# Optimization experiments

Hardware: AMD Instinct MI355X
Metric: run time of the kernel (lower is better)

Reference implementation:

```python
import jax, jax.numpy as jnp
import numpy as np

CAP = 15.0
EPS = 1e-6
NUM_HEADS = 16
HEAD_DIM = 64

def _rmsnorm(x, w):
    xf = x.astype(jnp.float32)
    var = jnp.mean(xf * xf, axis=-1, keepdims=True)
    return w * (xf * jax.lax.rsqrt(var + EPS)).astype(x.dtype)

def _gate(g):
    # sigmoid(soft_cap(g)) with cap 15
    return jax.nn.sigmoid(CAP * jnp.tanh(g / CAP))

def setup_inputs() -> dict:
    key = jax.random.key(0)
    ks = jax.random.split(key, 4)
    B, S, D = 4, 2048, 1024
    H, Dh = NUM_HEADS, HEAD_DIM
    return {
        "x": jax.random.normal(ks[0], (B, S, D), jnp.float32),
        "hidden_state": jnp.zeros((B, H, Dh, Dh), jnp.float32),
        "w_rms": jnp.ones((D,), jnp.float32),
        "w_qkv": jax.random.normal(ks[1], (D, 3 * H * Dh), jnp.float32) * 0.02,
        "w_gate": jax.random.normal(ks[2], (D, 3 * H), jnp.float32) * 0.02,
        "w_out": jax.random.normal(ks[3], (D, D), jnp.float32) * 0.02,
    }

def reference(x, hidden_state, w_rms, w_qkv, w_gate, w_out):
    B, S, D = x.shape
    H, Dh = NUM_HEADS, HEAD_DIM
    residual = x
    xn = _rmsnorm(x, w_rms)
    qkv = (xn @ w_qkv).reshape(B, S, 3, H, Dh)
    q, k, v = qkv[:, :, 0], qkv[:, :, 1], qkv[:, :, 2]  # [B,S,H,Dh]
    gates = _gate((xn @ w_gate).reshape(B, S, 3, H))
    i_g, f_g, o_g = gates[:, :, 0], gates[:, :, 1], gates[:, :, 2]  # [B,S,H]

    # time-major for scan: [S,B,H,...]
    def tm(a):
        return jnp.moveaxis(a, 1, 0)

    def step(state, inp):
        qt, kt, vt, it, ft, ot = inp  # [B,H,Dh]/[B,H]
        kv = kt[..., :, None] * vt[..., None, :]            # [B,H,Dh,Dh]
        state = ft[..., None, None] * state + it[..., None, None] * kv
        h = jnp.einsum('bhd,bhde->bhe', qt, state) * ot[..., None]
        return state, h

    _, h_seq = jax.lax.scan(step, hidden_state,
                            (tm(q), tm(k), tm(v), tm(i_g), tm(f_g), tm(o_g)))
    out = jnp.moveaxis(h_seq, 0, 1).reshape(B, S, H * Dh) @ w_out
    return residual + out
```

## Files before the change

kernel.cpp:

```cpp
#include <hip/hip_runtime.h>
#include <math.h>

typedef unsigned short u16;
typedef unsigned int   u32;
typedef __bf16 bf16x8 __attribute__((ext_vector_type(8)));
typedef float  f32x4  __attribute__((ext_vector_type(4)));

#define NBATCH 4
#define SEQ    2048
#define DIM    1024
#define NH     16
#define BH     64
#define NC     32
#define ROWS   8192
#define N1     3200

__device__ __forceinline__ u16 f2bf(float f) {
  u32 u = __builtin_bit_cast(u32, f);
  u32 r = u + 0x7fffu + ((u >> 16) & 1u);
  return (u16)(r >> 16);
}
__device__ __forceinline__ float bf2f(u16 h) {
  return __builtin_bit_cast(float, (u32)h << 16);
}

__device__ __forceinline__ void gl2lds16(const u16* g, u16* l) {
  __builtin_amdgcn_global_load_lds(
      (const __attribute__((address_space(1))) u32*)g,
      (__attribute__((address_space(3))) u32*)l, 16, 0, 0);
}

__global__ __launch_bounds__(256) void transpose_w(const float* __restrict__ W,
                                                   u16* __restrict__ Bt, int K, int N) {
  __shared__ float tile[32][33];
  const int n0 = blockIdx.x * 32, k0 = blockIdx.y * 32;
  const int tx = threadIdx.x, ty = threadIdx.y;
  #pragma unroll
  for (int i = 0; i < 4; i++)
    tile[ty + i * 8][tx] = W[(size_t)(k0 + ty + i * 8) * N + n0 + tx];
  __syncthreads();
  #pragma unroll
  for (int i = 0; i < 4; i++)
    Bt[(size_t)(n0 + ty + i * 8) * K + k0 + tx] = f2bf(tile[tx][ty + i * 8]);
}

__global__ __launch_bounds__(256) void fill_gateW(const float* __restrict__ wg,
                                                  u16* __restrict__ Bt) {
  const int g = blockIdx.x;
  const int tid = threadIdx.x;
  #pragma unroll
  for (int kk = 0; kk < 4; kk++) {
    const int k = kk * 256 + tid;
    u16 v = 0;
    if (g < 48) v = f2bf(wg[(size_t)k * 48 + g]);
    Bt[(size_t)(3072 + g) * 1024 + k] = v;
  }
}

__global__ __launch_bounds__(256) void rmsnorm_k(const float* __restrict__ x,
                                                 const float* __restrict__ w,
                                                 u16* __restrict__ xn) {
  const int row = blockIdx.x, tid = threadIdx.x;
  const float4 xv = *(const float4*)&x[(size_t)row * 1024 + tid * 4];
  float ss = xv.x * xv.x + xv.y * xv.y + xv.z * xv.z + xv.w * xv.w;
  #pragma unroll
  for (int off = 32; off > 0; off >>= 1) ss += __shfl_down(ss, off);
  __shared__ float red[4];
  if ((tid & 63) == 0) red[tid >> 6] = ss;
  __syncthreads();
  const float tot = red[0] + red[1] + red[2] + red[3];
  const float scale = rsqrtf(tot * (1.0f / 1024.0f) + 1e-6f);
  const float4 wv = *(const float4*)&w[tid * 4];
  const u16 o0 = f2bf(xv.x * scale * wv.x), o1 = f2bf(xv.y * scale * wv.y);
  const u16 o2 = f2bf(xv.z * scale * wv.z), o3 = f2bf(xv.w * scale * wv.w);
  uint2 ov;
  ov.x = (u32)o0 | ((u32)o1 << 16);
  ov.y = (u32)o2 | ((u32)o3 << 16);
  *(uint2*)&xn[(size_t)row * 1024 + tid * 4] = ov;
}

__device__ __forceinline__ void gemm_core256(const u16* __restrict__ A, const u16* __restrict__ Bt,
                                             int K, int rowBase, int colBase,
                                             u16* As, u16* Bs, f32x4 (&acc)[4][4]) {
  const int tid = threadIdx.x;
  const int lane = tid & 63;
  const int q = lane >> 4, m16 = lane & 15;
  const int wave = tid >> 6;
  const int wm = wave & 3, wn = wave >> 2;
  const u16* gA[4]; u16* lA[4];
  const u16* gB[2]; u16* lB[2];
  #pragma unroll
  for (int j = 0; j < 4; j++) {
    const int c = tid + j * 512;
    gA[j] = &A[(size_t)(rowBase + (c >> 3)) * K + (c & 7) * 8];
    lA[j] = As + c * 8;
  }
  #pragma unroll
  for (int j = 0; j < 2; j++) {
    const int c = tid + j * 512;
    gB[j] = &Bt[(size_t)(colBase + (c >> 3)) * K + (c & 7) * 8];
    lB[j] = Bs + c * 8;
  }
  for (int kb = 0; kb < K / 64; ++kb) {
    __syncthreads();
    #pragma unroll
    for (int j = 0; j < 4; j++) { gl2lds16(gA[j], lA[j]); gA[j] += 64; }
    #pragma unroll
    for (int j = 0; j < 2; j++) { gl2lds16(gB[j], lB[j]); gB[j] += 64; }
    __syncthreads();
    #pragma unroll
    for (int ks = 0; ks < 2; ks++) {
      bf16x8 af[4], bfr[4];
      #pragma unroll
      for (int mi = 0; mi < 4; mi++)
        af[mi] = *(const bf16x8*)&As[(wm * 64 + mi * 16 + m16) * 64 + ks * 32 + q * 8];
      #pragma unroll
      for (int ni = 0; ni < 4; ni++)
        bfr[ni] = *(const bf16x8*)&Bs[(wn * 64 + ni * 16 + m16) * 64 + ks * 32 + q * 8];
      #pragma unroll
      for (int mi = 0; mi < 4; mi++)
        #pragma unroll
        for (int ni = 0; ni < 4; ni++)
          acc[mi][ni] = __builtin_amdgcn_mfma_f32_16x16x32_bf16(af[mi], bfr[ni], acc[mi][ni], 0, 0, 0);
    }
  }
}

__device__ __forceinline__ void gemm_core128(const u16* __restrict__ A, const u16* __restrict__ Bt,
                                             int K, int rowBase, int colBase,
                                             u16* As, u16* Bs, f32x4 (&acc)[4][4]) {
  const int tid = threadIdx.x;
  const int lane = tid & 63;
  const int q = lane >> 4, m16 = lane & 15;
  const int wave = tid >> 6;
  const int wm = wave & 1, wn = wave >> 1;
  const u16* gA[4]; u16* lA[4];
  const u16* gB[4]; u16* lB[4];
  #pragma unroll
  for (int j = 0; j < 4; j++) {
    const int c = tid + j * 256;
    gA[j] = &A[(size_t)(rowBase + (c >> 3)) * K + (c & 7) * 8];
    lA[j] = As + c * 8;
    gB[j] = &Bt[(size_t)(colBase + (c >> 3)) * K + (c & 7) * 8];
    lB[j] = Bs + c * 8;
  }
  for (int kb = 0; kb < K / 64; ++kb) {
    __syncthreads();
    #pragma unroll
    for (int j = 0; j < 4; j++) { gl2lds16(gA[j], lA[j]); gA[j] += 64; }
    #pragma unroll
    for (int j = 0; j < 4; j++) { gl2lds16(gB[j], lB[j]); gB[j] += 64; }
    __syncthreads();
    #pragma unroll
    for (int ks = 0; ks < 2; ks++) {
      bf16x8 af[4], bfr[4];
      #pragma unroll
      for (int mi = 0; mi < 4; mi++)
        af[mi] = *(const bf16x8*)&As[(wm * 64 + mi * 16 + m16) * 64 + ks * 32 + q * 8];
      #pragma unroll
      for (int ni = 0; ni < 4; ni++)
        bfr[ni] = *(const bf16x8*)&Bs[(wn * 64 + ni * 16 + m16) * 64 + ks * 32 + q * 8];
      #pragma unroll
      for (int mi = 0; mi < 4; mi++)
        #pragma unroll
        for (int ni = 0; ni < 4; ni++)
          acc[mi][ni] = __builtin_amdgcn_mfma_f32_16x16x32_bf16(af[mi], bfr[ni], acc[mi][ni], 0, 0, 0);
    }
  }
}

__global__ __launch_bounds__(512, 4) void gemm_qkv(const u16* __restrict__ A, const u16* __restrict__ Bt,
                                                   u16* __restrict__ Qb, u16* __restrict__ Kb,
                                                   u16* __restrict__ Vb, float* __restrict__ gates) {
  __shared__ __attribute__((aligned(16))) u16 As[256 * 64];
  __shared__ __attribute__((aligned(16))) u16 Bs[128 * 64];
  f32x4 acc[4][4] = {};
  const int rowBase = blockIdx.x * 256, colBase = blockIdx.y * 128;
  gemm_core256(A, Bt, 1024, rowBase, colBase, As, Bs, acc);
  const int tid = threadIdx.x;
  const int lane = tid & 63, wave = tid >> 6;
  const int q = lane >> 4, m16 = lane & 15;
  const int wm = wave & 3, wn = wave >> 2;
  __syncthreads();
  if (colBase < 3072) {
    const int which = colBase >> 10;
    u16* dstBase = (which == 0) ? Qb : ((which == 1) ? Kb : Vb);
    const int b = rowBase >> 11;
    const int h = ((colBase & 1023) >> 6) + wn;
    const int tRow0 = (rowBase & 2047) + wm * 64;
    u16* scratch = As + wave * 1024;
    u16* headBase = dstBase + ((size_t)(b * 16 + h)) * 2048 * 64;
    const int rr = lane >> 2, co = (lane & 3) * 16;
    #pragma unroll
    for (int mi = 0; mi < 4; mi++) {
      #pragma unroll
      for (int ni = 0; ni < 4; ni++)
        #pragma unroll
        for (int r = 0; r < 4; r++)
          scratch[(q * 4 + r) * 64 + ni * 16 + m16] = f2bf(acc[mi][ni][r]);
      const uint4 d0 = *(const uint4*)&scratch[rr * 64 + co];
      const uint4 d1 = *(const uint4*)&scratch[rr * 64 + co + 8];
      u16* gp = headBase + (size_t)(tRow0 + mi * 16 + rr) * 64 + co;
      *(uint4*)gp = d0;
      *(uint4*)(gp + 8) = d1;
    }
  } else {
    #pragma unroll
    for (int ni = 0; ni < 4; ni++) {
      const int c2 = wn * 64 + ni * 16 + m16;
      if (c2 < 48) {
        const int which = c2 >> 4, hh = c2 & 15;
        #pragma unroll
        for (int mi = 0; mi < 4; mi++)
          #pragma unroll
          for (int r = 0; r < 4; r++) {
            const int grow = rowBase + wm * 64 + mi * 16 + q * 4 + r;
            const int b = grow >> 11, t = grow & 2047;
            const float v = acc[mi][ni][r];
            const float g = 1.0f / (1.0f + expf(-(15.0f * tanhf(v * (1.0f / 15.0f)))));
            gates[((size_t)which * 64 + (b * 16 + hh)) * 2048 + t] = g;
          }
      }
    }
  }
}

__global__ __launch_bounds__(256, 4) void gemm_out(const u16* __restrict__ A, const u16* __restrict__ Bt,
                                                   const float* __restrict__ resid,
                                                   float* __restrict__ out) {
  __shared__ __attribute__((aligned(16))) u16 As[128 * 64];
  __shared__ __attribute__((aligned(16))) u16 Bs[128 * 64];
  f32x4 acc[4][4] = {};
  const int rowBase = blockIdx.x * 128, colBase = blockIdx.y * 128;
  gemm_core128(A, Bt, 1024, rowBase, colBase, As, Bs, acc);
  const int tid = threadIdx.x;
  const int lane = tid & 63, wave = tid >> 6;
  const int q = lane >> 4, m16 = lane & 15;
  const int wm = wave & 1, wn = wave >> 1;
  #pragma unroll
  for (int mi = 0; mi < 4; mi++)
    #pragma unroll
    for (int ni = 0; ni < 4; ni++)
      #pragma unroll
      for (int r = 0; r < 4; r++) {
        const int grow = rowBase + wm * 64 + mi * 16 + q * 4 + r;
        const int gcol = colBase + wn * 64 + ni * 16 + m16;
        const size_t idx = (size_t)grow * 1024 + gcol;
        out[idx] = acc[mi][ni][r] + resid[idx];
      }
}

__global__ __launch_bounds__(64) void la_k(const float* __restrict__ gates,
                                           float* __restrict__ la) {
  const int bh = blockIdx.x >> 5, c = blockIdx.x & 31, lane = threadIdx.x;
  const int t = c * 64 + lane;
  float x = logf(gates[(size_t)(64 + bh) * 2048 + t]);
  #pragma unroll
  for (int off = 1; off < 64; off <<= 1) {
    const float y = __shfl_up(x, off);
    if (lane >= off) x += y;
  }
  la[(size_t)bh * 2048 + t] = x;
}

__global__ __launch_bounds__(256) void passA_k(const u16* __restrict__ Qb, const u16* __restrict__ Kb,
                                               const u16* __restrict__ Vb,
                                               const float* __restrict__ gates,
                                               const float* __restrict__ la,
                                               float* __restrict__ Mbuf, u16* __restrict__ hseq) {
  __shared__ u16 Ql[64][72], Kl[64][72], KTl[64][72], VTl[64][72], Pl[64][72];
  __shared__ float laS[64], iS[64];
  const int tid = threadIdx.x;
  const int bh = blockIdx.x >> 5, c = blockIdx.x & 31;
  const int lane = tid & 63, w = tid >> 6;
  const int q = lane >> 4, m16 = lane & 15;
  const size_t base = ((size_t)bh * 2048 + c * 64) * 64;
  const int tbase = bh * 2048 + c * 64;

  {
    const int s = tid >> 2, db = (tid & 3) * 16;
    if (tid < 64) {
      laS[tid] = la[tbase + tid];
      iS[tid] = gates[(size_t)bh * 2048 + c * 64 + tid];
    }
    const float la_s = la[tbase + s];
    const float i_s = gates[(size_t)bh * 2048 + c * 64 + s];
    const float la63 = la[tbase + 63];
    const float wk = expf(la63 - la_s) * i_s;
    const uint4 q0 = *(const uint4*)&Qb[base + s * 64 + db];
    const uint4 q1 = *(const uint4*)&Qb[base + s * 64 + db + 8];
    *(uint4*)&Ql[s][db] = q0;
    *(uint4*)&Ql[s][db + 8] = q1;
    const uint4 k0 = *(const uint4*)&Kb[base + s * 64 + db];
    const uint4 k1 = *(const uint4*)&Kb[base + s * 64 + db + 8];
    *(uint4*)&Kl[s][db] = k0;
    *(uint4*)&Kl[s][db + 8] = k1;
    u16 ktmp[16];
    *(uint4*)&ktmp[0] = k0;
    *(uint4*)&ktmp[8] = k1;
    #pragma unroll
    for (int j = 0; j < 16; j++) KTl[db + j][s] = f2bf(wk * bf2f(ktmp[j]));
    const uint4 v0 = *(const uint4*)&Vb[base + s * 64 + db];
    const uint4 v1 = *(const uint4*)&Vb[base + s * 64 + db + 8];
    u16 vtmp[16];
    *(uint4*)&vtmp[0] = v0;
    *(uint4*)&vtmp[8] = v1;
    #pragma unroll
    for (int j = 0; j < 16; j++) VTl[db + j][s] = vtmp[j];
  }
  __syncthreads();

  f32x4 pacc[4] = {};
  #pragma unroll
  for (int ks = 0; ks < 2; ks++) {
    const bf16x8 aq = *(const bf16x8*)&Ql[w * 16 + m16][ks * 32 + q * 8];
    #pragma unroll
    for (int ni = 0; ni < 4; ni++) {
      const bf16x8 bk = *(const bf16x8*)&Kl[ni * 16 + m16][ks * 32 + q * 8];
      pacc[ni] = __builtin_amdgcn_mfma_f32_16x16x32_bf16(aq, bk, pacc[ni], 0, 0, 0);
    }
  }
  #pragma unroll
  for (int ni = 0; ni < 4; ni++)
    #pragma unroll
    for (int r = 0; r < 4; r++) {
      const int tt = w * 16 + q * 4 + r, ss = ni * 16 + m16;
      float Wts = 0.0f;
      if (ss <= tt) Wts = expf(laS[tt] - laS[ss]) * iS[ss];
      Pl[tt][ss] = f2bf(pacc[ni][r] * Wts);
    }
  __syncthreads();

  f32x4 hacc[4] = {}, macc[4] = {};
  #pragma unroll
  for (int ks = 0; ks < 2; ks++) {
    const bf16x8 ap = *(const bf16x8*)&Pl[w * 16 + m16][ks * 32 + q * 8];
    const bf16x8 ak = *(const bf16x8*)&KTl[w * 16 + m16][ks * 32 + q * 8];
    #pragma unroll
    for (int ni = 0; ni < 4; ni++) {
      const bf16x8 bv = *(const bf16x8*)&VTl[ni * 16 + m16][ks * 32 + q * 8];
      hacc[ni] = __builtin_amdgcn_mfma_f32_16x16x32_bf16(ap, bv, hacc[ni], 0, 0, 0);
      macc[ni] = __builtin_amdgcn_mfma_f32_16x16x32_bf16(ak, bv, macc[ni], 0, 0, 0);
    }
  }
  const int b = bh >> 4, h = bh & 15;
  #pragma unroll
  for (int ni = 0; ni < 4; ni++)
    #pragma unroll
    for (int r = 0; r < 4; r++) {
      const int tt = w * 16 + q * 4 + r, e = ni * 16 + m16;
      const int tg = c * 64 + tt;
      hseq[((size_t)b * 2048 + tg) * 1024 + h * 64 + e] = f2bf(hacc[ni][r]);
      Mbuf[(((size_t)bh * 32 + c) * 64 + tt) * 64 + e] = macc[ni][r];
    }
}

__global__ __launch_bounds__(256) void passB_k(float* __restrict__ Mbuf,
                                               const float* __restrict__ hidden,
                                               const float* __restrict__ la) {
  const int bh = blockIdx.x >> 4;
  const int e = (blockIdx.x & 15) * 256 + threadIdx.x;
  __shared__ float Gs[32];
  if (threadIdx.x < 32)
    Gs[threadIdx.x] = expf(la[(size_t)bh * 2048 + threadIdx.x * 64 + 63]);
  __syncthreads();
  float st = hidden[(size_t)bh * 4096 + e];
  float* M = &Mbuf[(size_t)bh * 32 * 4096 + e];
  float m_next = M[0];
  #pragma unroll 4
  for (int c = 0; c < 32; c++) {
    const float m_cur = m_next;
    if (c < 31) m_next = M[(size_t)(c + 1) * 4096];
    M[(size_t)c * 4096] = st;
    st = Gs[c] * st + m_cur;
  }
}

__global__ __launch_bounds__(256) void passC_k(const u16* __restrict__ Qb,
                                               const float* __restrict__ Sprev,
                                               const float* __restrict__ la,
                                               const float* __restrict__ gates,
                                               u16* __restrict__ hseq) {
  __shared__ u16 aQl[64][72], STl[64][72];
  const int tid = threadIdx.x;
  const int bh = blockIdx.x >> 5, c = blockIdx.x & 31;
  const int lane = tid & 63, w = tid >> 6;
  const int q = lane >> 4, m16 = lane & 15;
  const size_t base = ((size_t)bh * 2048 + c * 64) * 64;
  const int tbase = bh * 2048 + c * 64;
  {
    const int s = tid >> 2, db = (tid & 3) * 16;
    const float a_s = expf(la[tbase + s]);
    const uint4 q0 = *(const uint4*)&Qb[base + s * 64 + db];
    const uint4 q1 = *(const uint4*)&Qb[base + s * 64 + db + 8];
    u16 qtmp[16];
    *(uint4*)&qtmp[0] = q0;
    *(uint4*)&qtmp[8] = q1;
    #pragma unroll
    for (int j = 0; j < 16; j++) aQl[s][db + j] = f2bf(a_s * bf2f(qtmp[j]));
    const float* Sp = &Sprev[((size_t)bh * 32 + c) * 4096];
    #pragma unroll
    for (int j = 0; j < 16; j++) STl[db + j][s] = f2bf(Sp[s * 64 + db + j]);
  }
  __syncthreads();
  f32x4 acc[4] = {};
  #pragma unroll
  for (int ks = 0; ks < 2; ks++) {
    const bf16x8 a = *(const bf16x8*)&aQl[w * 16 + m16][ks * 32 + q * 8];
    #pragma unroll
    for (int ni = 0; ni < 4; ni++) {
      const bf16x8 bb = *(const bf16x8*)&STl[ni * 16 + m16][ks * 32 + q * 8];
      acc[ni] = __builtin_amdgcn_mfma_f32_16x16x32_bf16(a, bb, acc[ni], 0, 0, 0);
    }
  }
  const int b = bh >> 4, h = bh & 15;
  #pragma unroll
  for (int ni = 0; ni < 4; ni++)
    #pragma unroll
    for (int r = 0; r < 4; r++) {
      const int tt = w * 16 + q * 4 + r, e = ni * 16 + m16;
      const int tg = c * 64 + tt;
      const float o = gates[(size_t)(128 + bh) * 2048 + tg];
      const size_t idx = ((size_t)b * 2048 + tg) * 1024 + h * 64 + e;
      hseq[idx] = f2bf(o * (bf2f(hseq[idx]) + acc[ni][r]));
    }
}

extern "C" void kernel_launch(void* const* d_in, const int* in_sizes, int n_in,
                              void* d_out, int out_size, void* d_ws, size_t ws_size,
                              hipStream_t stream) {
  (void)in_sizes; (void)n_in; (void)out_size; (void)ws_size;
  const float* x      = (const float*)d_in[0];
  const float* hidden = (const float*)d_in[1];
  const float* w_rms  = (const float*)d_in[2];
  const float* w_qkv  = (const float*)d_in[3];
  const float* w_gate = (const float*)d_in[4];
  const float* w_out  = (const float*)d_in[5];
  float* out = (float*)d_out;

  char* p = (char*)d_ws;
  u16* wqkvT = (u16*)p;  p += (size_t)N1 * 1024 * 2;
  u16* woutT = (u16*)p;  p += (size_t)1024 * 1024 * 2;
  u16* xn    = (u16*)p;  p += (size_t)ROWS * 1024 * 2;
  u16* Qb    = (u16*)p;  p += (size_t)BH * 2048 * 64 * 2;
  u16* Kb    = (u16*)p;  p += (size_t)BH * 2048 * 64 * 2;
  u16* Vb    = (u16*)p;  p += (size_t)BH * 2048 * 64 * 2;
  float* gates = (float*)p; p += (size_t)3 * BH * 2048 * 4;
  float* la    = (float*)p; p += (size_t)BH * 2048 * 4;
  float* Mbuf  = (float*)p; p += (size_t)BH * NC * 4096 * 4;
  u16* hseq  = (u16*)p;  p += (size_t)ROWS * 1024 * 2;

  transpose_w<<<dim3(96, 32), dim3(32, 8), 0, stream>>>(w_qkv, wqkvT, 1024, 3072);
  transpose_w<<<dim3(32, 32), dim3(32, 8), 0, stream>>>(w_out, woutT, 1024, 1024);
  fill_gateW<<<128, 256, 0, stream>>>(w_gate, wqkvT);
  rmsnorm_k<<<ROWS, 256, 0, stream>>>(x, w_rms, xn);
  gemm_qkv<<<dim3(32, 25), 512, 0, stream>>>(xn, wqkvT, Qb, Kb, Vb, gates);
  la_k<<<BH * NC, 64, 0, stream>>>(gates, la);
  passA_k<<<BH * NC, 256, 0, stream>>>(Qb, Kb, Vb, gates, la, Mbuf, hseq);
  passB_k<<<BH * 16, 256, 0, stream>>>(Mbuf, hidden, la);
  passC_k<<<BH * NC, 256, 0, stream>>>(Qb, Mbuf, la, gates, hseq);
  gemm_out<<<dim3(64, 8), 256, 0, stream>>>(hseq, woutT, x, out);
}
```

Baseline: 289.1 us.

## Split GEMM LDS tiles into K-halves and fold log-gate scan into passA

The GEMM cores now store the 64-wide K tile in LDS as two 32-wide halves, each row 64 bytes, instead of one 128-byte row. This changes the bank mapping of the MFMA fragment reads and is meant to reduce LDS bank conflicts. Separately, the per-chunk log-cumsum of the forget gates is computed inside passA, which still writes it out for later passes, so the standalone la_k launch is removed. The cost is an extra __syncthreads at the start of passA and a short serial prologue there.

```diff
diff --git a/kernel.cpp b/kernel.cpp
--- a/kernel.cpp
+++ b/kernel.cpp
@@ -92,13 +92,15 @@
   #pragma unroll
   for (int j = 0; j < 4; j++) {
     const int c = tid + j * 512;
-    gA[j] = &A[(size_t)(rowBase + (c >> 3)) * K + (c & 7) * 8];
+    const int half = c >> 10, cc = c & 1023;
+    gA[j] = &A[(size_t)(rowBase + (cc >> 2)) * K + half * 32 + (cc & 3) * 8];
     lA[j] = As + c * 8;
   }
   #pragma unroll
   for (int j = 0; j < 2; j++) {
     const int c = tid + j * 512;
-    gB[j] = &Bt[(size_t)(colBase + (c >> 3)) * K + (c & 7) * 8];
+    const int half = c >> 9, cc = c & 511;
+    gB[j] = &Bt[(size_t)(colBase + (cc >> 2)) * K + half * 32 + (cc & 3) * 8];
     lB[j] = Bs + c * 8;
   }
   for (int kb = 0; kb < K / 64; ++kb) {
@@ -110,13 +112,15 @@
     __syncthreads();
     #pragma unroll
     for (int ks = 0; ks < 2; ks++) {
+      const int aoff = ks * 8192;
+      const int boff = ks * 4096;
       bf16x8 af[4], bfr[4];
       #pragma unroll
       for (int mi = 0; mi < 4; mi++)
-        af[mi] = *(const bf16x8*)&As[(wm * 64 + mi * 16 + m16) * 64 + ks * 32 + q * 8];
+        af[mi] = *(const bf16x8*)&As[aoff + (wm * 64 + mi * 16 + m16) * 32 + q * 8];
       #pragma unroll
       for (int ni = 0; ni < 4; ni++)
-        bfr[ni] = *(const bf16x8*)&Bs[(wn * 64 + ni * 16 + m16) * 64 + ks * 32 + q * 8];
+        bfr[ni] = *(const bf16x8*)&Bs[boff + (wn * 64 + ni * 16 + m16) * 32 + q * 8];
       #pragma unroll
       for (int mi = 0; mi < 4; mi++)
         #pragma unroll
@@ -139,9 +143,10 @@
   #pragma unroll
   for (int j = 0; j < 4; j++) {
     const int c = tid + j * 256;
-    gA[j] = &A[(size_t)(rowBase + (c >> 3)) * K + (c & 7) * 8];
+    const int half = c >> 9, cc = c & 511;
+    gA[j] = &A [(size_t)(rowBase + (cc >> 2)) * K + half * 32 + (cc & 3) * 8];
     lA[j] = As + c * 8;
-    gB[j] = &Bt[(size_t)(colBase + (c >> 3)) * K + (c & 7) * 8];
+    gB[j] = &Bt[(size_t)(colBase + (cc >> 2)) * K + half * 32 + (cc & 3) * 8];
     lB[j] = Bs + c * 8;
   }
   for (int kb = 0; kb < K / 64; ++kb) {
@@ -153,13 +158,14 @@
     __syncthreads();
     #pragma unroll
     for (int ks = 0; ks < 2; ks++) {
+      const int off = ks * 4096;
       bf16x8 af[4], bfr[4];
       #pragma unroll
       for (int mi = 0; mi < 4; mi++)
-        af[mi] = *(const bf16x8*)&As[(wm * 64 + mi * 16 + m16) * 64 + ks * 32 + q * 8];
+        af[mi] = *(const bf16x8*)&As[off + (wm * 64 + mi * 16 + m16) * 32 + q * 8];
       #pragma unroll
       for (int ni = 0; ni < 4; ni++)
-        bfr[ni] = *(const bf16x8*)&Bs[(wn * 64 + ni * 16 + m16) * 64 + ks * 32 + q * 8];
+        bfr[ni] = *(const bf16x8*)&Bs[off + (wn * 64 + ni * 16 + m16) * 32 + q * 8];
       #pragma unroll
       for (int mi = 0; mi < 4; mi++)
         #pragma unroll
@@ -250,23 +256,10 @@
       }
 }
 
-__global__ __launch_bounds__(64) void la_k(const float* __restrict__ gates,
-                                           float* __restrict__ la) {
-  const int bh = blockIdx.x >> 5, c = blockIdx.x & 31, lane = threadIdx.x;
-  const int t = c * 64 + lane;
-  float x = logf(gates[(size_t)(64 + bh) * 2048 + t]);
-  #pragma unroll
-  for (int off = 1; off < 64; off <<= 1) {
-    const float y = __shfl_up(x, off);
-    if (lane >= off) x += y;
-  }
-  la[(size_t)bh * 2048 + t] = x;
-}
-
 __global__ __launch_bounds__(256) void passA_k(const u16* __restrict__ Qb, const u16* __restrict__ Kb,
                                                const u16* __restrict__ Vb,
                                                const float* __restrict__ gates,
-                                               const float* __restrict__ la,
+                                               float* __restrict__ la,
                                                float* __restrict__ Mbuf, u16* __restrict__ hseq) {
   __shared__ u16 Ql[64][72], Kl[64][72], KTl[64][72], VTl[64][72], Pl[64][72];
   __shared__ float laS[64], iS[64];
@@ -275,18 +268,24 @@
   const int lane = tid & 63, w = tid >> 6;
   const int q = lane >> 4, m16 = lane & 15;
   const size_t base = ((size_t)bh * 2048 + c * 64) * 64;
-  const int tbase = bh * 2048 + c * 64;
+  const int toff = c * 64;
+
+  if (tid < 64) {
+    float lg = logf(gates[(size_t)(64 + bh) * 2048 + toff + tid]);
+    #pragma unroll
+    for (int off = 1; off < 64; off <<= 1) {
+      const float y = __shfl_up(lg, off);
+      if (tid >= off) lg += y;
+    }
+    laS[tid] = lg;
+    iS[tid] = gates[(size_t)bh * 2048 + toff + tid];
+    la[(size_t)bh * 2048 + toff + tid] = lg;
+  }
+  __syncthreads();
 
   {
     const int s = tid >> 2, db = (tid & 3) * 16;
-    if (tid < 64) {
-      laS[tid] = la[tbase + tid];
-      iS[tid] = gates[(size_t)bh * 2048 + c * 64 + tid];
-    }
-    const float la_s = la[tbase + s];
-    const float i_s = gates[(size_t)bh * 2048 + c * 64 + s];
-    const float la63 = la[tbase + 63];
-    const float wk = expf(la63 - la_s) * i_s;
+    const float wk = expf(laS[63] - laS[s]) * iS[s];
     const uint4 q0 = *(const uint4*)&Qb[base + s * 64 + db];
     const uint4 q1 = *(const uint4*)&Qb[base + s * 64 + db + 8];
     *(uint4*)&Ql[s][db] = q0;
@@ -455,7 +454,6 @@
   fill_gateW<<<128, 256, 0, stream>>>(w_gate, wqkvT);
   rmsnorm_k<<<ROWS, 256, 0, stream>>>(x, w_rms, xn);
   gemm_qkv<<<dim3(32, 25), 512, 0, stream>>>(xn, wqkvT, Qb, Kb, Vb, gates);
-  la_k<<<BH * NC, 64, 0, stream>>>(gates, la);
   passA_k<<<BH * NC, 256, 0, stream>>>(Qb, Kb, Vb, gates, la, Mbuf, hseq);
   passB_k<<<BH * 16, 256, 0, stream>>>(Mbuf, hidden, la);
   passC_k<<<BH * NC, 256, 0, stream>>>(Qb, Mbuf, la, gates, hseq);
```

New measurement: 268.1 us. 1.08x faster.
